# Optimization experiments

Measured on AMD Instinct MI355X. Metric: run time of the kernel, lower is better.

Reference implementation:

```python
import jax, jax.numpy as jnp
import numpy as np

B, QL, T, H = 32, 1, 2048, 512


def setup_inputs() -> dict:
    key = jax.random.key(0)
    ks = jax.random.split(key, 10)
    n = lambda i, shape, sc=1.0: jax.random.normal(ks[i], shape, dtype=jnp.float32) * sc
    inv = 1.0 / np.sqrt(H)
    return {
        "query": n(0, (B, QL, H)),
        "value": n(1, (B, T, H)),
        "last_attn": jax.random.uniform(ks[2], (B, T), dtype=jnp.float32),
        "conv_w": n(3, (H, 1, 3), 0.1),   # Conv1d weight (out_ch, in_ch=1, k=3)
        "conv_b": n(4, (H,), 0.1),
        "q_w": n(5, (H, H), inv),          # query_proj (no bias)
        "v_w": n(6, (H, H), inv),          # value_proj (no bias)
        "s_w": n(7, (1, H), inv),          # score_proj weight
        "s_b": n(8, (1,), 0.1),            # score_proj bias
        "bias": n(9, (H,), 0.1),           # learned additive bias
    }


def reference(query, value, last_attn, conv_w, conv_b, q_w, v_w, s_w, s_b, bias):
    Tlen = last_attn.shape[1]
    # Conv1d(in=1, out=H, k=3, pad=1) over last_attn, then transpose -> (B, T, H)
    pad = jnp.pad(last_attn, ((0, 0), (1, 1)))
    frames = jnp.stack([pad[:, k:k + Tlen] for k in range(3)], axis=0)  # (3, B, T)
    conv_attn = jnp.einsum('hk,kbt->bth', conv_w[:, 0, :], frames) + conv_b  # (B, T, H)
    q = jnp.einsum('bqh,oh->bqo', query, q_w)   # (B, 1, H)
    v = jnp.einsum('bth,oh->bto', value, v_w)   # (B, T, H)
    e = jnp.tanh(q + v + conv_attn + bias)      # (B, T, H), q broadcasts over T
    score = jnp.einsum('bth,oh->bt', e, s_w) + s_b  # (B, T)
    # smoothing=True branch: sigmoid then L1-normalize
    score = jax.nn.sigmoid(score)
    attn = score / jnp.sum(score, axis=-1, keepdims=True)
    context = jnp.einsum('bt,bth->bh', attn, value)  # bmm(attn[:,None,:], value).squeeze(1)
    return context, attn
```

## Files before the change

kernel.cpp:

```cpp
#include <hip/hip_runtime.h>
#include <math.h>

#define B 32
#define T 2048
#define H 512

#define BT2 64
#define ASTR 520

typedef __attribute__((ext_vector_type(8))) __bf16 bf16x8;
typedef __attribute__((ext_vector_type(4))) __bf16 bf16x4v;
typedef __attribute__((ext_vector_type(4))) float f32x4;
typedef __attribute__((ext_vector_type(4))) float floatx4;

union pack8 { bf16x4v h; uint2 u; };

__global__ __launch_bounds__(256) void k_init(const float* __restrict__ query,
                                              const float* __restrict__ q_w,
                                              const float* __restrict__ bias,
                                              const float* __restrict__ v_w,
                                              float* __restrict__ qpb,
                                              unsigned short* __restrict__ wbf,
                                              float* __restrict__ ctx_num,
                                              float* __restrict__ denom) {
    const int blk = blockIdx.x;
    const int tid = threadIdx.x;

    if (blk >= 544) {
#pragma unroll
        for (int i = 0; i < 16; ++i) {
            const int off = tid * 4 + i * 1024;
            *(f32x4*)(ctx_num + off) = (f32x4){0.f, 0.f, 0.f, 0.f};
        }
        if (tid < B) denom[tid] = 0.f;
        return;
    }
    if (blk >= 512) {
        const int c2 = blk - 512;
        const int wv = tid >> 6;
        const int lane = tid & 63;
        const int srow = (c2 >> 2) * 64 + (c2 & 3) * 16 + (lane & 15);
        const int scol0 = (lane >> 4) * 8;
#pragma unroll
        for (int kk = 0; kk < 4; ++kk) {
            const int k = wv * 4 + kk;
            const float* src = v_w + (size_t)srow * H + k * 32 + scol0;
            f32x4 a0 = *(const f32x4*)src;
            f32x4 a1 = *(const f32x4*)(src + 4);
            pack8 p0, p1;
            p0.h = __builtin_convertvector(a0, bf16x4v);
            p1.h = __builtin_convertvector(a1, bf16x4v);
            uint4 u = {p0.u.x, p0.u.y, p1.u.x, p1.u.y};
            *(uint4*)(wbf + ((size_t)c2 * 16 + k) * 512 + lane * 8) = u;
        }
        return;
    }

    const int b = blk >> 4;
    const int s = blk & 15;
    const int wave = tid >> 6;
    const int lane = tid & 63;

    const float* qb = query + (size_t)b * H + lane * 8;
    float4 q0 = *(const float4*)qb;
    float4 q1 = *(const float4*)(qb + 4);

    const int o0 = s * 32 + wave * 8;
#pragma unroll
    for (int i = 0; i < 8; ++i) {
        const int o = o0 + i;
        const float* wr = q_w + (size_t)o * H + lane * 8;
        float4 w0 = *(const float4*)wr;
        float4 w1 = *(const float4*)(wr + 4);
        float acc = w0.x * q0.x + w0.y * q0.y + w0.z * q0.z + w0.w * q0.w +
                    w1.x * q1.x + w1.y * q1.y + w1.z * q1.z + w1.w * q1.w;
#pragma unroll
        for (int m = 1; m < 64; m <<= 1) acc += __shfl_xor(acc, m);
        if (lane == 0) qpb[b * H + o] = acc + bias[o];
    }
}

__global__ __launch_bounds__(512, 4) void k2_fused(const float* __restrict__ value,
                                                   const unsigned short* __restrict__ wbf,
                                                   const float* __restrict__ la,
                                                   const float* __restrict__ conv_w,
                                                   const float* __restrict__ conv_b,
                                                   const float* __restrict__ s_w,
                                                   const float* __restrict__ qpb,
                                                   const float* __restrict__ s_b,
                                                   float* __restrict__ pre_sg,
                                                   float* __restrict__ ctx_num,
                                                   float* __restrict__ denom) {
    __shared__ __align__(16) unsigned short As[BT2 * ASTR];
    __shared__ float las[BT2 + 2];
    __shared__ float redp[BT2][9];
    __shared__ float sgs[BT2];
    __shared__ float redc[4][H];

    const int t0 = blockIdx.x * BT2;
    const int b  = blockIdx.y;
    const int tid = threadIdx.x;
    const int wave = tid >> 6;
    const int lane = tid & 63;
    const int tx   = lane & 15;
    const int quad = lane >> 4;
    const int wn   = wave * 64;

    if (tid < BT2 + 2) {
        const int t = t0 + tid - 1;
        las[tid] = (t >= 0 && t < T) ? la[b * T + t] : 0.f;
    }

    {
        const int srow = tid >> 3;
        const int scol = (tid & 7) * 8;
        const float* sg = value + ((size_t)b * T + t0 + srow) * H + scol;
        unsigned short* sl = &As[srow * ASTR + scol];
#pragma unroll
        for (int c = 0; c < 8; ++c) {
            f32x4 a0 = *(const f32x4*)(sg + c * 64);
            f32x4 a1 = *(const f32x4*)(sg + c * 64 + 4);
            pack8 p0, p1;
            p0.h = __builtin_convertvector(a0, bf16x4v);
            p1.h = __builtin_convertvector(a1, bf16x4v);
            uint4 u = {p0.u.x, p0.u.y, p1.u.x, p1.u.y};
            *(uint4*)(sl + c * 64) = u;
        }
    }
    __syncthreads();

    floatx4 acc[4][4];
#pragma unroll
    for (int i = 0; i < 4; ++i)
#pragma unroll
        for (int j = 0; j < 4; ++j) acc[i][j] = (floatx4){0.f, 0.f, 0.f, 0.f};

    const unsigned short* gB = wbf + (size_t)wave * 32768 + lane * 8;
    const unsigned short* aB = &As[tx * ASTR + quad * 8];

    bf16x8 bcur[4], bnxt[4];
#pragma unroll
    for (int ni = 0; ni < 4; ++ni)
        bcur[ni] = *(const bf16x8*)(gB + ni * 8192);

#pragma unroll
    for (int k = 0; k < 16; ++k) {
        if (k < 15) {
#pragma unroll
            for (int ni = 0; ni < 4; ++ni)
                bnxt[ni] = *(const bf16x8*)(gB + ni * 8192 + (k + 1) * 512);
        }
        bf16x8 af[4];
#pragma unroll
        for (int mi = 0; mi < 4; ++mi)
            af[mi] = *(const bf16x8*)(aB + mi * 16 * ASTR + k * 32);
#pragma unroll
        for (int mi = 0; mi < 4; ++mi)
#pragma unroll
            for (int ni = 0; ni < 4; ++ni)
                acc[mi][ni] = __builtin_amdgcn_mfma_f32_16x16x32_bf16(
                    af[mi], bcur[ni], acc[mi][ni], 0, 0, 0);
        if (k < 15) {
#pragma unroll
            for (int ni = 0; ni < 4; ++ni) bcur[ni] = bnxt[ni];
        }
    }

    float qp4[4], sw4[4], cb4[4], c04[4], c14[4], c24[4];
#pragma unroll
    for (int ni = 0; ni < 4; ++ni) {
        const int ol = wn + ni * 16 + tx;
        qp4[ni] = qpb[b * H + ol];
        sw4[ni] = s_w[ol];
        cb4[ni] = conv_b[ol];
        c04[ni] = conv_w[ol * 3 + 0];
        c14[ni] = conv_w[ol * 3 + 1];
        c24[ni] = conv_w[ol * 3 + 2];
    }

    float sacc[16];
#pragma unroll
    for (int i = 0; i < 16; ++i) sacc[i] = 0.f;
#pragma unroll
    for (int ni = 0; ni < 4; ++ni) {
#pragma unroll
        for (int mi = 0; mi < 4; ++mi)
#pragma unroll
            for (int r = 0; r < 4; ++r) {
                const int tl = mi * 16 + quad * 4 + r;
                const float conv = c04[ni] * las[tl] + c14[ni] * las[tl + 1] +
                                   c24[ni] * las[tl + 2] + cb4[ni];
                const float x = acc[mi][ni][r] + qp4[ni] + conv;
                const float ex = __expf(2.f * x);
                const float th = 1.f - 2.f * __builtin_amdgcn_rcpf(ex + 1.f);
                sacc[mi * 4 + r] += sw4[ni] * th;
            }
    }
#pragma unroll
    for (int i = 0; i < 16; ++i) {
        float v = sacc[i];
        v += __shfl_xor(v, 1);
        v += __shfl_xor(v, 2);
        v += __shfl_xor(v, 4);
        v += __shfl_xor(v, 8);
        if (tx == 0) redp[(i >> 2) * 16 + quad * 4 + (i & 3)][wave] = v;
    }
    __syncthreads();

    if (tid < BT2) {
        float sc = s_b[0];
#pragma unroll
        for (int w = 0; w < 8; ++w) sc += redp[tid][w];
        const float sg = 1.f / (1.f + __expf(-sc));
        sgs[tid] = sg;
        pre_sg[b * T + t0 + tid] = sg;
        float dsum = sg;
#pragma unroll
        for (int m = 1; m < 64; m <<= 1) dsum += __shfl_xor(dsum, m);
        if (tid == 0) atomicAdd(&denom[b], dsum);
    }
    __syncthreads();

    {
        const int h4 = (tid & 127) * 4;
        const int tp = tid >> 7;
        f32x4 a = {0.f, 0.f, 0.f, 0.f};
        for (int t = tp; t < BT2; t += 4) {
            const float w = sgs[t];
            bf16x4v hv = *(const bf16x4v*)&As[t * ASTR + h4];
            f32x4 v = __builtin_convertvector(hv, f32x4);
            a.x += w * v.x; a.y += w * v.y; a.z += w * v.z; a.w += w * v.w;
        }
        *(f32x4*)&redc[tp][h4] = a;
    }
    __syncthreads();
    if (tid < 128) {
        const int h = tid * 4;
        f32x4 r0 = *(const f32x4*)&redc[0][h];
        f32x4 r1 = *(const f32x4*)&redc[1][h];
        f32x4 r2 = *(const f32x4*)&redc[2][h];
        f32x4 r3 = *(const f32x4*)&redc[3][h];
        atomicAdd(&ctx_num[b * H + h + 0], r0.x + r1.x + r2.x + r3.x);
        atomicAdd(&ctx_num[b * H + h + 1], r0.y + r1.y + r2.y + r3.y);
        atomicAdd(&ctx_num[b * H + h + 2], r0.z + r1.z + r2.z + r3.z);
        atomicAdd(&ctx_num[b * H + h + 3], r0.w + r1.w + r2.w + r3.w);
    }
}

__global__ __launch_bounds__(256) void k3_scale(const float* __restrict__ pre_sg,
                                                const float* __restrict__ ctx_num,
                                                const float* __restrict__ denom,
                                                float* __restrict__ attn_out,
                                                float* __restrict__ ctx) {
    const int bx = blockIdx.x;
    const int b  = blockIdx.y;
    const int tid = threadIdx.x;
    const float inv = 1.f / denom[b];
    const int t = bx * 256 + tid;
    attn_out[b * T + t] = pre_sg[b * T + t] * inv;
    if (tid < 64) {
        const int h = bx * 64 + tid;
        ctx[b * H + h] = ctx_num[b * H + h] * inv;
    }
}

extern "C" void kernel_launch(void* const* d_in, const int* in_sizes, int n_in,
                              void* d_out, int out_size, void* d_ws, size_t ws_size,
                              hipStream_t stream) {
    const float* query  = (const float*)d_in[0];
    const float* value  = (const float*)d_in[1];
    const float* la     = (const float*)d_in[2];
    const float* conv_w = (const float*)d_in[3];
    const float* conv_b = (const float*)d_in[4];
    const float* q_w    = (const float*)d_in[5];
    const float* v_w    = (const float*)d_in[6];
    const float* s_w    = (const float*)d_in[7];
    const float* s_b    = (const float*)d_in[8];
    const float* bias   = (const float*)d_in[9];

    float* out  = (float*)d_out;
    float* ctx  = out;
    float* attn = out + B * H;

    float* qpb     = (float*)d_ws;
    float* pre_sg  = qpb + B * H;
    float* ctx_num = pre_sg + B * T;
    float* denom   = ctx_num + B * H;
    unsigned short* wbf = (unsigned short*)(denom + 64);

    k_init<<<545, 256, 0, stream>>>(query, q_w, bias, v_w, qpb, wbf, ctx_num, denom);

    dim3 g2(T / BT2, B);
    k2_fused<<<g2, 512, 0, stream>>>(value, wbf, la, conv_w, conv_b, s_w, qpb, s_b,
                                     pre_sg, ctx_num, denom);

    dim3 g3(8, B);
    k3_scale<<<g3, 256, 0, stream>>>(pre_sg, ctx_num, denom, attn, ctx);
}
```

Measured before the change: 251.7 us.

## Double time tile to 128 rows and overlap value staging with MFMA

Doubles the per-block time tile from 64 to 128 rows, so each block reuses each bf16 weight fragment it loads from global memory across twice as many MFMA rows, halving weight traffic per output. Value staging into LDS is split into four column chunks: the first is converted up front and later chunks are loaded into registers while MFMAs on earlier chunks run, with a barrier after each chunk. The cost is roughly doubled accumulator registers and LDS use (occupancy bound lowered to 2), and the denominator atomic now fires per wave because 128 rows span two waves.

```diff
diff --git a/kernel.cpp b/kernel.cpp
--- a/kernel.cpp
+++ b/kernel.cpp
@@ -5,7 +5,7 @@
 #define T 2048
 #define H 512
 
-#define BT2 64
+#define BT2 128
 #define ASTR 520
 
 typedef __attribute__((ext_vector_type(8))) __bf16 bf16x8;
@@ -80,7 +80,7 @@
     }
 }
 
-__global__ __launch_bounds__(512, 4) void k2_fused(const float* __restrict__ value,
+__global__ __launch_bounds__(512, 2) void k2_fused(const float* __restrict__ value,
                                                    const unsigned short* __restrict__ wbf,
                                                    const float* __restrict__ la,
                                                    const float* __restrict__ conv_w,
@@ -111,32 +111,35 @@
         las[tid] = (t >= 0 && t < T) ? la[b * T + t] : 0.f;
     }
 
+    const int srow = tid >> 2;
+    const int scol = (tid & 3) * 32;
+    const float* sgp = value + ((size_t)b * T + t0 + srow) * H + scol;
+    unsigned short* slp = &As[srow * ASTR + scol];
+
     {
-        const int srow = tid >> 3;
-        const int scol = (tid & 7) * 8;
-        const float* sg = value + ((size_t)b * T + t0 + srow) * H + scol;
-        unsigned short* sl = &As[srow * ASTR + scol];
-#pragma unroll
-        for (int c = 0; c < 8; ++c) {
-            f32x4 a0 = *(const f32x4*)(sg + c * 64);
-            f32x4 a1 = *(const f32x4*)(sg + c * 64 + 4);
+        f32x4 r[8];
+#pragma unroll
+        for (int i = 0; i < 8; ++i) r[i] = *(const f32x4*)(sgp + i * 4);
+#pragma unroll
+        for (int i = 0; i < 4; ++i) {
             pack8 p0, p1;
-            p0.h = __builtin_convertvector(a0, bf16x4v);
-            p1.h = __builtin_convertvector(a1, bf16x4v);
+            p0.h = __builtin_convertvector(r[2 * i], bf16x4v);
+            p1.h = __builtin_convertvector(r[2 * i + 1], bf16x4v);
             uint4 u = {p0.u.x, p0.u.y, p1.u.x, p1.u.y};
-            *(uint4*)(sl + c * 64) = u;
+            *(uint4*)(slp + i * 8) = u;
         }
     }
     __syncthreads();
 
-    floatx4 acc[4][4];
-#pragma unroll
-    for (int i = 0; i < 4; ++i)
+    floatx4 acc[8][4];
+#pragma unroll
+    for (int i = 0; i < 8; ++i)
 #pragma unroll
         for (int j = 0; j < 4; ++j) acc[i][j] = (floatx4){0.f, 0.f, 0.f, 0.f};
 
     const unsigned short* gB = wbf + (size_t)wave * 32768 + lane * 8;
-    const unsigned short* aB = &As[tx * ASTR + quad * 8];
+    const unsigned short* aBlo = &As[tx * ASTR + quad * 8];
+    const unsigned short* aBhi = aBlo + 64 * ASTR;
 
     bf16x8 bcur[4], bnxt[4];
 #pragma unroll
@@ -144,25 +147,51 @@
         bcur[ni] = *(const bf16x8*)(gB + ni * 8192);
 
 #pragma unroll
-    for (int k = 0; k < 16; ++k) {
-        if (k < 15) {
-#pragma unroll
-            for (int ni = 0; ni < 4; ++ni)
-                bnxt[ni] = *(const bf16x8*)(gB + ni * 8192 + (k + 1) * 512);
-        }
-        bf16x8 af[4];
-#pragma unroll
-        for (int mi = 0; mi < 4; ++mi)
-            af[mi] = *(const bf16x8*)(aB + mi * 16 * ASTR + k * 32);
-#pragma unroll
-        for (int mi = 0; mi < 4; ++mi)
-#pragma unroll
-            for (int ni = 0; ni < 4; ++ni)
-                acc[mi][ni] = __builtin_amdgcn_mfma_f32_16x16x32_bf16(
-                    af[mi], bcur[ni], acc[mi][ni], 0, 0, 0);
-        if (k < 15) {
-#pragma unroll
-            for (int ni = 0; ni < 4; ++ni) bcur[ni] = bnxt[ni];
+    for (int c = 0; c < 4; ++c) {
+        f32x4 srg[8];
+        if (c < 3) {
+#pragma unroll
+            for (int i = 0; i < 8; ++i)
+                srg[i] = *(const f32x4*)(sgp + (c + 1) * 128 + i * 4);
+        }
+
+#pragma unroll
+        for (int kk = 0; kk < 4; ++kk) {
+            const int k = c * 4 + kk;
+            if (k < 15) {
+#pragma unroll
+                for (int ni = 0; ni < 4; ++ni)
+                    bnxt[ni] = *(const bf16x8*)(gB + ni * 8192 + (k + 1) * 512);
+            }
+            bf16x8 af[8];
+#pragma unroll
+            for (int mi = 0; mi < 4; ++mi)
+                af[mi] = *(const bf16x8*)(aBlo + mi * 16 * ASTR + k * 32);
+#pragma unroll
+            for (int mi = 0; mi < 4; ++mi)
+                af[mi + 4] = *(const bf16x8*)(aBhi + mi * 16 * ASTR + k * 32);
+#pragma unroll
+            for (int mi = 0; mi < 8; ++mi)
+#pragma unroll
+                for (int ni = 0; ni < 4; ++ni)
+                    acc[mi][ni] = __builtin_amdgcn_mfma_f32_16x16x32_bf16(
+                        af[mi], bcur[ni], acc[mi][ni], 0, 0, 0);
+            if (k < 15) {
+#pragma unroll
+                for (int ni = 0; ni < 4; ++ni) bcur[ni] = bnxt[ni];
+            }
+        }
+
+        if (c < 3) {
+#pragma unroll
+            for (int i = 0; i < 4; ++i) {
+                pack8 p0, p1;
+                p0.h = __builtin_convertvector(srg[2 * i], bf16x4v);
+                p1.h = __builtin_convertvector(srg[2 * i + 1], bf16x4v);
+                uint4 u = {p0.u.x, p0.u.y, p1.u.x, p1.u.y};
+                *(uint4*)(slp + (c + 1) * 128 + i * 8) = u;
+            }
+            __syncthreads();
         }
     }
 
@@ -178,13 +207,13 @@
         c24[ni] = conv_w[ol * 3 + 2];
     }
 
-    float sacc[16];
-#pragma unroll
-    for (int i = 0; i < 16; ++i) sacc[i] = 0.f;
+    float sacc[32];
+#pragma unroll
+    for (int i = 0; i < 32; ++i) sacc[i] = 0.f;
 #pragma unroll
     for (int ni = 0; ni < 4; ++ni) {
 #pragma unroll
-        for (int mi = 0; mi < 4; ++mi)
+        for (int mi = 0; mi < 8; ++mi)
 #pragma unroll
             for (int r = 0; r < 4; ++r) {
                 const int tl = mi * 16 + quad * 4 + r;
@@ -197,7 +226,7 @@
             }
     }
 #pragma unroll
-    for (int i = 0; i < 16; ++i) {
+    for (int i = 0; i < 32; ++i) {
         float v = sacc[i];
         v += __shfl_xor(v, 1);
         v += __shfl_xor(v, 2);
@@ -217,7 +246,7 @@
         float dsum = sg;
 #pragma unroll
         for (int m = 1; m < 64; m <<= 1) dsum += __shfl_xor(dsum, m);
-        if (tid == 0) atomicAdd(&denom[b], dsum);
+        if (lane == 0) atomicAdd(&denom[b], dsum);
     }
     __syncthreads();
 
```

After: 254.8 us. No clear change (+1.2%).
